# Performance work log

Hardware: AMD Instinct MI355X
Metric: run time of the kernel (lower is better)

## Reference

```python
import jax, jax.numpy as jnp
import numpy as np

TOKENS, D_IN, D_OUT, RANK = 16384, 4096, 4096, 512

def setup_inputs() -> dict:
    key = jax.random.key(0)
    k1, k2, k3, k4 = jax.random.split(key, 4)
    x = jax.random.normal(k1, (TOKENS, D_IN), dtype=jnp.float32)
    U = jax.random.normal(k2, (D_OUT, RANK), dtype=jnp.float32) * 0.02
    sigma = jax.random.uniform(k3, (RANK,), dtype=jnp.float32)
    V = jax.random.normal(k4, (D_IN, RANK), dtype=jnp.float32) * 0.02
    return {"x": x, "U": U, "sigma": sigma, "V": V}

def reference(x, U, sigma, V):
    # W = U @ diag(sigma) @ V.T  (shape [out, in]); out = x @ W.T
    # diag(sigma) contraction expressed as a column scale of U (same math).
    W = (U * sigma[None, :]) @ V.T          # [out, in]
    return x @ W.T                          # [tokens, out]
```

## Files before the change

### kernel.cpp

```cpp
#include <hip/hip_runtime.h>

typedef __bf16 bf16;
typedef __bf16 bf16x4 __attribute__((ext_vector_type(4)));
typedef __bf16 bf16x8 __attribute__((ext_vector_type(8)));
typedef float  f32x4  __attribute__((ext_vector_type(4)));

#define TOKENS 16384
#define D_IN   4096
#define D_OUT  4096
#define RANK   512

__device__ inline void gload_lds16(const void* g, void* l) {
    __builtin_amdgcn_global_load_lds((const __attribute__((address_space(1))) void*)g,
                                     (__attribute__((address_space(3))) void*)l,
                                     16, 0, 0);
}

__global__ __launch_bounds__(256) void vt_scale(const float* __restrict__ V,
                                                const float* __restrict__ sg,
                                                bf16* __restrict__ Vst) {
    __shared__ float tile[64][65];
    const int tx = threadIdx.x & 63;
    const int ty = threadIdx.x >> 6;
    const int kb = blockIdx.x * 64;
    const int rb = blockIdx.y * 64;
    const float s = sg[rb + tx];
#pragma unroll
    for (int i = ty; i < 64; i += 4)
        tile[i][tx] = V[(size_t)(kb + i) * RANK + rb + tx] * s;
    __syncthreads();
#pragma unroll
    for (int i = ty; i < 64; i += 4) {
        int r = rb + i;
        int kp = kb + (tx ^ ((r & 7) << 3));
        Vst[(size_t)r * D_IN + kp] = (bf16)tile[tx][i];
    }
}

__global__ __launch_bounds__(256) void cvt_u_swz(const float* __restrict__ U,
                                                 bf16* __restrict__ Ub) {
    int g = blockIdx.x * 256 + threadIdx.x;
    int n = g >> 6;
    int c = g & 63;
    int blk = c >> 3, q = c & 7;
    const float* src = U + (size_t)n * RANK + c * 8;
    f32x4 v0 = *(const f32x4*)src;
    f32x4 v1 = *(const f32x4*)(src + 4);
    bf16x8 b;
    b[0] = (bf16)v0[0]; b[1] = (bf16)v0[1]; b[2] = (bf16)v0[2]; b[3] = (bf16)v0[3];
    b[4] = (bf16)v1[0]; b[5] = (bf16)v1[1]; b[6] = (bf16)v1[2]; b[7] = (bf16)v1[3];
    *(bf16x8*)(Ub + (size_t)n * RANK + blk * 64 + ((q ^ (n & 7)) * 8)) = b;
}

__device__ inline bf16x8 cvt8(f32x4 a, f32x4 b) {
    bf16x8 r;
    r[0] = (bf16)a[0]; r[1] = (bf16)a[1]; r[2] = (bf16)a[2]; r[3] = (bf16)a[3];
    r[4] = (bf16)b[0]; r[5] = (bf16)b[1]; r[6] = (bf16)b[2]; r[7] = (bf16)b[3];
    return r;
}

__global__ __launch_bounds__(256) void gemm1_alds(const float* __restrict__ A,
                                                  const bf16* __restrict__ B,
                                                  bf16* __restrict__ T,
                                                  int M, int N, int K) {
    __shared__ float Afl[128 * 64];
    __shared__ bf16  Bl[128 * 64];

    const int t  = threadIdx.x;
    const int l  = t & 63;
    const int w  = t >> 6;
    const int wr = w >> 1, wc = w & 1;
    const int lr = l & 15;
    const int kg = l >> 4;
    const int sxorB = (lr & 7) << 3;

    const int nwg = gridDim.x;
    const int bid = blockIdx.x;
    const int cpx = nwg >> 3;
    const int swz = (bid & 7) * cpx + (bid >> 3);
    const int ntn = N >> 7;
    const int tm  = (swz / ntn) << 7;
    const int tn  = (swz % ntn) << 7;

    const int arow = t >> 4;
    const int acr  = t & 15;
    const float* Asrc = A + (size_t)(tm + arow) * K + ((acr ^ arow) << 2);
    const bf16* Bp = B + (size_t)(tn + (t >> 3)) * K + (t & 7) * 8;

    f32x4 acc[4][4] = {};

    for (int kt = 0; kt < K; kt += 64) {
#pragma unroll
        for (int c = 0; c < 8; ++c)
            gload_lds16(Asrc + kt + (size_t)(c * 16) * K, &Afl[(c * 256 + t) * 4]);
#pragma unroll
        for (int c = 0; c < 4; ++c)
            gload_lds16(Bp + kt + (size_t)(c * 32) * K, &Bl[(c * 256 + t) * 8]);
        __syncthreads();

#pragma unroll
        for (int ks = 0; ks < 2; ++ks) {
            bf16x8 af[4], bfr[4];
            const int q0 = ks * 8 + kg * 2;
#pragma unroll
            for (int f = 0; f < 4; ++f) {
                const float* Arow = &Afl[(wr * 64 + f * 16 + lr) * 64];
                f32x4 h0 = *(const f32x4*)&Arow[(q0 ^ lr) << 2];
                f32x4 h1 = *(const f32x4*)&Arow[((q0 + 1) ^ lr) << 2];
                af[f] = cvt8(h0, h1);
                bfr[f] = *(const bf16x8*)&Bl[(wc * 64 + f * 16 + lr) * 64 +
                                             ((ks * 32 + kg * 8) ^ sxorB)];
            }
#pragma unroll
            for (int fm = 0; fm < 4; ++fm)
#pragma unroll
                for (int fn = 0; fn < 4; ++fn)
                    acc[fm][fn] = __builtin_amdgcn_mfma_f32_16x16x32_bf16(
                        af[fm], bfr[fn], acc[fm][fn], 0, 0, 0);
        }
        __syncthreads();
    }

    const int r0 = tm + wr * 64 + kg * 4;
    const int c0 = tn + wc * 64 + lr;
#pragma unroll
    for (int fm = 0; fm < 4; ++fm)
#pragma unroll
        for (int fn = 0; fn < 4; ++fn)
#pragma unroll
            for (int r = 0; r < 4; ++r) {
                int row = r0 + fm * 16 + r;
                int col = (c0 + fn * 16) ^ ((row & 7) << 3);
                T[(size_t)row * N + col] = (bf16)acc[fm][fn][r];
            }
}

__global__ __launch_bounds__(512, 2) void gemm2_8p(const bf16* __restrict__ A,
                                                   const bf16* __restrict__ B,
                                                   float* __restrict__ out,
                                                   int M, int N, int K) {
    __shared__ bf16 Al[2][256 * 64];
    __shared__ bf16 Bl[2][256 * 64];

    const int t   = threadIdx.x;
    const int l   = t & 63;
    const int wid = t >> 6;
    const int wm  = wid >> 2;
    const int wn  = wid & 3;
    const int lr  = l & 15;
    const int kg  = l >> 4;
    const int sxor = (lr & 7) << 3;

    const int nwg = gridDim.x;
    const int bid = blockIdx.x;
    const int cpx = nwg >> 3;
    const int swz = (bid & 7) * cpx + (bid >> 3);
    const int ntn = N >> 8;
    const int tm  = (swz / ntn) << 8;
    const int tn  = (swz % ntn) << 8;

    const bf16* Apt = A + (size_t)(tm + (t >> 3)) * K + (t & 7) * 8;
    const bf16* Bpt = B + (size_t)(tn + (t >> 3)) * K + (t & 7) * 8;
    const int ldst = t * 8;

    const int NT = K >> 6;

    f32x4 acc[8][4] = {};
    bf16x8 aq[4][2], bq[2][2];

#define STAGE(BUF, KT)                                                         \
    _Pragma("unroll") for (int c = 0; c < 4; ++c) {                            \
        gload_lds16(Apt + (KT) + (size_t)(c * 64) * K, &Al[BUF][c * 4096 + ldst]); \
        gload_lds16(Bpt + (KT) + (size_t)(c * 64) * K, &Bl[BUF][c * 4096 + ldst]); \
    }

#define RD_A(BUF, QM)                                                          \
    _Pragma("unroll") for (int f = 0; f < 4; ++f)                              \
    _Pragma("unroll") for (int ks = 0; ks < 2; ++ks)                           \
        aq[f][ks] = *(const bf16x8*)&Al[BUF][(wm * 128 + (QM) * 64 + f * 16 + lr) * 64 + \
                                            ((ks * 32 + kg * 8) ^ sxor)];

#define RD_B(BUF, QN)                                                          \
    _Pragma("unroll") for (int f = 0; f < 2; ++f)                              \
    _Pragma("unroll") for (int ks = 0; ks < 2; ++ks)                           \
        bq[f][ks] = *(const bf16x8*)&Bl[BUF][(wn * 64 + (QN) * 32 + f * 16 + lr) * 64 + \
                                            ((ks * 32 + kg * 8) ^ sxor)];

#define MM(QM, QN)                                                             \
    __builtin_amdgcn_s_setprio(1);                                             \
    _Pragma("unroll") for (int ks = 0; ks < 2; ++ks)                           \
    _Pragma("unroll") for (int fm = 0; fm < 4; ++fm)                           \
    _Pragma("unroll") for (int fn = 0; fn < 2; ++fn)                           \
        acc[(QM) * 4 + fm][(QN) * 2 + fn] = __builtin_amdgcn_mfma_f32_16x16x32_bf16( \
            aq[fm][ks], bq[fn][ks], acc[(QM) * 4 + fm][(QN) * 2 + fn], 0, 0, 0); \
    __builtin_amdgcn_s_setprio(0);

    STAGE(0, 0);
    STAGE(1, 64);
    asm volatile("s_waitcnt vmcnt(8)" ::: "memory");
    __builtin_amdgcn_sched_barrier(0);
    __builtin_amdgcn_s_barrier();
    __builtin_amdgcn_sched_barrier(0);

    for (int i = 0; i < NT; ++i) {
        const int p = i & 1;
        RD_A(p, 0); RD_B(p, 0); MM(0, 0);
        RD_B(p, 1);             MM(0, 1);
        RD_A(p, 1); RD_B(p, 0); MM(1, 0);
        RD_B(p, 1);             MM(1, 1);

        if (i + 1 < NT) {
            __builtin_amdgcn_sched_barrier(0);
            __builtin_amdgcn_s_barrier();
            __builtin_amdgcn_sched_barrier(0);
            if (i + 2 < NT) {
                STAGE(p, (i + 2) * 64);
                asm volatile("s_waitcnt vmcnt(8)" ::: "memory");
            } else {
                asm volatile("s_waitcnt vmcnt(0)" ::: "memory");
            }
            __builtin_amdgcn_sched_barrier(0);
            __builtin_amdgcn_s_barrier();
            __builtin_amdgcn_sched_barrier(0);
        }
    }

    const int r0 = tm + wm * 128 + kg * 4;
    const int c0 = tn + wn * 64 + lr;
#pragma unroll
    for (int fm = 0; fm < 8; ++fm)
#pragma unroll
        for (int fn = 0; fn < 4; ++fn)
#pragma unroll
            for (int r = 0; r < 4; ++r)
                out[(size_t)(r0 + fm * 16 + r) * N + (c0 + fn * 16)] = acc[fm][fn][r];

#undef STAGE
#undef RD_A
#undef RD_B
#undef MM
}

extern "C" void kernel_launch(void* const* d_in, const int* in_sizes, int n_in,
                              void* d_out, int out_size, void* d_ws, size_t ws_size,
                              hipStream_t stream) {
    const float* x  = (const float*)d_in[0];
    const float* U  = (const float*)d_in[1];
    const float* sg = (const float*)d_in[2];
    const float* V  = (const float*)d_in[3];
    float* out = (float*)d_out;

    char* ws = (char*)d_ws;
    bf16* Vst = (bf16*)ws;
    bf16* Ub  = (bf16*)(ws + (4u << 20));
    bf16* T   = (bf16*)(ws + (8u << 20));

    vt_scale<<<dim3(D_IN / 64, RANK / 64), 256, 0, stream>>>(V, sg, Vst);
    cvt_u_swz<<<(D_OUT * RANK / 8) / 256, 256, 0, stream>>>(U, Ub);

    gemm1_alds<<<(TOKENS / 128) * (RANK / 128), 256, 0, stream>>>(
        x, Vst, T, TOKENS, RANK, D_IN);

    gemm2_8p<<<(TOKENS / 256) * (D_OUT / 256), 512, 0, stream>>>(
        T, Ub, out, TOKENS, D_OUT, RANK);
}
```

Before: 250.8 us.

## Rewrite first GEMM as double-buffered 8-wave kernel with 128x256 tiles

Replaces the 4-wave, single-buffered 128x128 first GEMM (x·V·sigma) with an 8-wave kernel that uses a 128x256 tile and double-buffered LDS. Loads for tile i+2 are issued while tile i is computed, with explicit vmcnt waits and barriers, and MFMA blocks run at raised wave priority. The goal is to hide global-load latency and halve the number of times the fp32 x tile is re-read across N. In exchange, LDS use grows to about 96KB, which limits residency to one block per CU, and the grid shrinks to 256 blocks.

```diff
diff --git a/kernel.cpp b/kernel.cpp
--- a/kernel.cpp
+++ b/kernel.cpp
@@ -14,6 +14,13 @@
     __builtin_amdgcn_global_load_lds((const __attribute__((address_space(1))) void*)g,
                                      (__attribute__((address_space(3))) void*)l,
                                      16, 0, 0);
+}
+
+__device__ inline bf16x8 cvt8(f32x4 a, f32x4 b) {
+    bf16x8 r;
+    r[0] = (bf16)a[0]; r[1] = (bf16)a[1]; r[2] = (bf16)a[2]; r[3] = (bf16)a[3];
+    r[4] = (bf16)b[0]; r[5] = (bf16)b[1]; r[6] = (bf16)b[2]; r[7] = (bf16)b[3];
+    return r;
 }
 
 __global__ __launch_bounds__(256) void vt_scale(const float* __restrict__ V,
@@ -52,77 +59,103 @@
     *(bf16x8*)(Ub + (size_t)n * RANK + blk * 64 + ((q ^ (n & 7)) * 8)) = b;
 }
 
-__device__ inline bf16x8 cvt8(f32x4 a, f32x4 b) {
-    bf16x8 r;
-    r[0] = (bf16)a[0]; r[1] = (bf16)a[1]; r[2] = (bf16)a[2]; r[3] = (bf16)a[3];
-    r[4] = (bf16)b[0]; r[5] = (bf16)b[1]; r[6] = (bf16)b[2]; r[7] = (bf16)b[3];
-    return r;
-}
-
-__global__ __launch_bounds__(256) void gemm1_alds(const float* __restrict__ A,
-                                                  const bf16* __restrict__ B,
-                                                  bf16* __restrict__ T,
-                                                  int M, int N, int K) {
-    __shared__ float Afl[128 * 64];
-    __shared__ bf16  Bl[128 * 64];
-
-    const int t  = threadIdx.x;
-    const int l  = t & 63;
-    const int w  = t >> 6;
-    const int wr = w >> 1, wc = w & 1;
-    const int lr = l & 15;
-    const int kg = l >> 4;
+__global__ __launch_bounds__(512, 1) void gemm1_8p(const float* __restrict__ A,
+                                                   const bf16* __restrict__ B,
+                                                   bf16* __restrict__ T,
+                                                   int M, int N, int K) {
+    __shared__ float Afl[2][128 * 64];
+    __shared__ bf16  Bl[2][256 * 64];
+
+    const int t   = threadIdx.x;
+    const int l   = t & 63;
+    const int wid = t >> 6;
+    const int wm  = wid >> 2;
+    const int wn  = wid & 3;
+    const int lr  = l & 15;
+    const int kg  = l >> 4;
     const int sxorB = (lr & 7) << 3;
 
     const int nwg = gridDim.x;
     const int bid = blockIdx.x;
     const int cpx = nwg >> 3;
     const int swz = (bid & 7) * cpx + (bid >> 3);
-    const int ntn = N >> 7;
+    const int ntn = N >> 8;
     const int tm  = (swz / ntn) << 7;
-    const int tn  = (swz % ntn) << 7;
+    const int tn  = (swz % ntn) << 8;
 
     const int arow = t >> 4;
     const int acr  = t & 15;
-    const float* Asrc = A + (size_t)(tm + arow) * K + ((acr ^ arow) << 2);
+    const float* Asrc = A + (size_t)(tm + arow) * K + ((acr ^ (arow & 15)) << 2);
     const bf16* Bp = B + (size_t)(tn + (t >> 3)) * K + (t & 7) * 8;
 
+    const int NT = K >> 6;
+
     f32x4 acc[4][4] = {};
-
-    for (int kt = 0; kt < K; kt += 64) {
-#pragma unroll
-        for (int c = 0; c < 8; ++c)
-            gload_lds16(Asrc + kt + (size_t)(c * 16) * K, &Afl[(c * 256 + t) * 4]);
-#pragma unroll
-        for (int c = 0; c < 4; ++c)
-            gload_lds16(Bp + kt + (size_t)(c * 32) * K, &Bl[(c * 256 + t) * 8]);
-        __syncthreads();
-
-#pragma unroll
-        for (int ks = 0; ks < 2; ++ks) {
-            bf16x8 af[4], bfr[4];
-            const int q0 = ks * 8 + kg * 2;
-#pragma unroll
-            for (int f = 0; f < 4; ++f) {
-                const float* Arow = &Afl[(wr * 64 + f * 16 + lr) * 64];
-                f32x4 h0 = *(const f32x4*)&Arow[(q0 ^ lr) << 2];
-                f32x4 h1 = *(const f32x4*)&Arow[((q0 + 1) ^ lr) << 2];
-                af[f] = cvt8(h0, h1);
-                bfr[f] = *(const bf16x8*)&Bl[(wc * 64 + f * 16 + lr) * 64 +
-                                             ((ks * 32 + kg * 8) ^ sxorB)];
+    bf16x8 aq[2][2], bq[2][2];
+
+#define STAGE1(BUF, KT)                                                        \
+    _Pragma("unroll") for (int c = 0; c < 4; ++c) {                            \
+        gload_lds16(Asrc + (KT) + (size_t)(c * 32) * K, &Afl[BUF][(c * 512 + t) * 4]); \
+        gload_lds16(Bp   + (KT) + (size_t)(c * 64) * K, &Bl[BUF][(c * 512 + t) * 8]);  \
+    }
+
+#define RD_A1(BUF, QM)                                                         \
+    _Pragma("unroll") for (int f = 0; f < 2; ++f)                              \
+    _Pragma("unroll") for (int ks = 0; ks < 2; ++ks) {                         \
+        const float* Arow = &Afl[BUF][(wm * 64 + ((QM) * 2 + f) * 16 + lr) * 64]; \
+        const int q0 = ks * 8 + kg * 2;                                        \
+        f32x4 h0 = *(const f32x4*)&Arow[(q0 ^ lr) << 2];                       \
+        f32x4 h1 = *(const f32x4*)&Arow[((q0 + 1) ^ lr) << 2];                 \
+        aq[f][ks] = cvt8(h0, h1);                                              \
+    }
+
+#define RD_B1(BUF, QN)                                                         \
+    _Pragma("unroll") for (int f = 0; f < 2; ++f)                              \
+    _Pragma("unroll") for (int ks = 0; ks < 2; ++ks)                           \
+        bq[f][ks] = *(const bf16x8*)&Bl[BUF][(wn * 64 + ((QN) * 2 + f) * 16 + lr) * 64 + \
+                                            ((ks * 32 + kg * 8) ^ sxorB)];
+
+#define MM1(QM, QN)                                                            \
+    __builtin_amdgcn_s_setprio(1);                                             \
+    _Pragma("unroll") for (int ks = 0; ks < 2; ++ks)                           \
+    _Pragma("unroll") for (int f = 0; f < 2; ++f)                              \
+    _Pragma("unroll") for (int g = 0; g < 2; ++g)                              \
+        acc[(QM) * 2 + f][(QN) * 2 + g] = __builtin_amdgcn_mfma_f32_16x16x32_bf16( \
+            aq[f][ks], bq[g][ks], acc[(QM) * 2 + f][(QN) * 2 + g], 0, 0, 0);   \
+    __builtin_amdgcn_s_setprio(0);
+
+    STAGE1(0, 0);
+    STAGE1(1, 64);
+    asm volatile("s_waitcnt vmcnt(8)" ::: "memory");
+    __builtin_amdgcn_sched_barrier(0);
+    __builtin_amdgcn_s_barrier();
+    __builtin_amdgcn_sched_barrier(0);
+
+    for (int i = 0; i < NT; ++i) {
+        const int p = i & 1;
+        RD_A1(p, 0); RD_B1(p, 0); MM1(0, 0);
+        RD_B1(p, 1);              MM1(0, 1);
+        RD_A1(p, 1); RD_B1(p, 0); MM1(1, 0);
+        RD_B1(p, 1);              MM1(1, 1);
+
+        if (i + 1 < NT) {
+            __builtin_amdgcn_sched_barrier(0);
+            __builtin_amdgcn_s_barrier();
+            __builtin_amdgcn_sched_barrier(0);
+            if (i + 2 < NT) {
+                STAGE1(p, (i + 2) * 64);
+                asm volatile("s_waitcnt vmcnt(8)" ::: "memory");
+            } else {
+                asm volatile("s_waitcnt vmcnt(0)" ::: "memory");
             }
-#pragma unroll
-            for (int fm = 0; fm < 4; ++fm)
-#pragma unroll
-                for (int fn = 0; fn < 4; ++fn)
-                    acc[fm][fn] = __builtin_amdgcn_mfma_f32_16x16x32_bf16(
-                        af[fm], bfr[fn], acc[fm][fn], 0, 0, 0);
+            __builtin_amdgcn_sched_barrier(0);
+            __builtin_amdgcn_s_barrier();
+            __builtin_amdgcn_sched_barrier(0);
         }
-        __syncthreads();
-    }
-
-    const int r0 = tm + wr * 64 + kg * 4;
-    const int c0 = tn + wc * 64 + lr;
+    }
+
+    const int r0 = tm + wm * 64 + kg * 4;
+    const int c0 = tn + wn * 64 + lr;
 #pragma unroll
     for (int fm = 0; fm < 4; ++fm)
 #pragma unroll
@@ -133,6 +166,10 @@
                 int col = (c0 + fn * 16) ^ ((row & 7) << 3);
                 T[(size_t)row * N + col] = (bf16)acc[fm][fn][r];
             }
+#undef STAGE1
+#undef RD_A1
+#undef RD_B1
+#undef MM1
 }
 
 __global__ __launch_bounds__(512, 2) void gemm2_8p(const bf16* __restrict__ A,
@@ -258,7 +295,7 @@
     vt_scale<<<dim3(D_IN / 64, RANK / 64), 256, 0, stream>>>(V, sg, Vst);
     cvt_u_swz<<<(D_OUT * RANK / 8) / 256, 256, 0, stream>>>(U, Ub);
 
-    gemm1_alds<<<(TOKENS / 128) * (RANK / 128), 256, 0, stream>>>(
+    gemm1_8p<<<(TOKENS / 128) * (RANK / 256), 512, 0, stream>>>(
         x, Vst, T, TOKENS, RANK, D_IN);
 
     gemm2_8p<<<(TOKENS / 256) * (D_OUT / 256), 512, 0, stream>>>(
```

After: 269.8 us. 7.6% more time.

## Split-K gemm1 with 256x256 tiles, bf16 LDS staging and separate reduction

Applied to the files above, without the earlier changes.

Replaces the 128x128 first GEMM with a 256x256-tile, 512-thread kernel that splits K=4096 into four 1024-wide slices. Each slice writes a bf16 partial product, and a new reduce kernel sums the partials and writes the swizzled T layout. The x tile is now loaded through registers and converted to bf16 once before the LDS store, instead of being staged as fp32 and converted on every fragment read. This raises per-tile data reuse and keeps the grid large, at the cost of extra partial-buffer traffic, an additional launch, and summing bf16-rounded partials.

```diff
diff --git a/kernel.cpp b/kernel.cpp
--- a/kernel.cpp
+++ b/kernel.cpp
@@ -52,87 +52,107 @@
     *(bf16x8*)(Ub + (size_t)n * RANK + blk * 64 + ((q ^ (n & 7)) * 8)) = b;
 }
 
-__device__ inline bf16x8 cvt8(f32x4 a, f32x4 b) {
-    bf16x8 r;
-    r[0] = (bf16)a[0]; r[1] = (bf16)a[1]; r[2] = (bf16)a[2]; r[3] = (bf16)a[3];
-    r[4] = (bf16)b[0]; r[5] = (bf16)b[1]; r[6] = (bf16)b[2]; r[7] = (bf16)b[3];
-    return r;
-}
-
-__global__ __launch_bounds__(256) void gemm1_alds(const float* __restrict__ A,
-                                                  const bf16* __restrict__ B,
-                                                  bf16* __restrict__ T,
-                                                  int M, int N, int K) {
-    __shared__ float Afl[128 * 64];
-    __shared__ bf16  Bl[128 * 64];
-
-    const int t  = threadIdx.x;
-    const int l  = t & 63;
-    const int w  = t >> 6;
-    const int wr = w >> 1, wc = w & 1;
-    const int lr = l & 15;
-    const int kg = l >> 4;
-    const int sxorB = (lr & 7) << 3;
+__global__ __launch_bounds__(512) void gemm1_v2(const float* __restrict__ A,
+                                                const bf16* __restrict__ B,
+                                                bf16* __restrict__ P,
+                                                int M, int N, int Kfull) {
+    __shared__ bf16 Al[256 * 64];
+    __shared__ bf16 Bl[256 * 64];
+
+    const int t   = threadIdx.x;
+    const int l   = t & 63;
+    const int wid = t >> 6;
+    const int wm  = wid >> 2;
+    const int wn  = wid & 3;
+    const int lr  = l & 15;
+    const int kg  = l >> 4;
 
     const int nwg = gridDim.x;
     const int bid = blockIdx.x;
     const int cpx = nwg >> 3;
     const int swz = (bid & 7) * cpx + (bid >> 3);
-    const int ntn = N >> 7;
-    const int tm  = (swz / ntn) << 7;
-    const int tn  = (swz % ntn) << 7;
+    const int split = swz >> 7;
+    const int tile  = swz & 127;
+    const int tm    = (tile >> 1) << 8;
+    const int tn    = (tile & 1) << 8;
+    const int kbase = split << 10;
+    const int Ks    = 1024;
 
     const int arow = t >> 4;
-    const int acr  = t & 15;
-    const float* Asrc = A + (size_t)(tm + arow) * K + ((acr ^ arow) << 2);
-    const bf16* Bp = B + (size_t)(tn + (t >> 3)) * K + (t & 7) * 8;
-
-    f32x4 acc[4][4] = {};
-
-    for (int kt = 0; kt < K; kt += 64) {
+    const int acg  = t & 15;
+    const float* Ap = A + (size_t)(tm + arow) * Kfull + kbase + acg * 4;
+    const int awo = (((acg >> 1) ^ (arow & 7)) << 3) + ((acg & 1) << 2);
+    const bf16* Bp = B + (size_t)(tn + (t >> 3)) * Kfull + kbase + (t & 7) * 8;
+
+    f32x4 acc[8][4] = {};
+
+    for (int kt = 0; kt < Ks; kt += 64) {
+#pragma unroll
+        for (int c = 0; c < 4; ++c)
+            gload_lds16(Bp + kt + (size_t)(c * 64) * Kfull, &Bl[(c * 512 + t) * 8]);
+        f32x4 ra[8];
 #pragma unroll
         for (int c = 0; c < 8; ++c)
-            gload_lds16(Asrc + kt + (size_t)(c * 16) * K, &Afl[(c * 256 + t) * 4]);
-#pragma unroll
-        for (int c = 0; c < 4; ++c)
-            gload_lds16(Bp + kt + (size_t)(c * 32) * K, &Bl[(c * 256 + t) * 8]);
+            ra[c] = *(const f32x4*)(Ap + kt + (size_t)(c * 32) * Kfull);
+#pragma unroll
+        for (int c = 0; c < 8; ++c) {
+            bf16x4 b = { (bf16)ra[c][0], (bf16)ra[c][1], (bf16)ra[c][2], (bf16)ra[c][3] };
+            *(bf16x4*)&Al[(c * 32 + arow) * 64 + awo] = b;
+        }
         __syncthreads();
 
 #pragma unroll
         for (int ks = 0; ks < 2; ++ks) {
-            bf16x8 af[4], bfr[4];
-            const int q0 = ks * 8 + kg * 2;
-#pragma unroll
-            for (int f = 0; f < 4; ++f) {
-                const float* Arow = &Afl[(wr * 64 + f * 16 + lr) * 64];
-                f32x4 h0 = *(const f32x4*)&Arow[(q0 ^ lr) << 2];
-                f32x4 h1 = *(const f32x4*)&Arow[((q0 + 1) ^ lr) << 2];
-                af[f] = cvt8(h0, h1);
-                bfr[f] = *(const bf16x8*)&Bl[(wc * 64 + f * 16 + lr) * 64 +
-                                             ((ks * 32 + kg * 8) ^ sxorB)];
-            }
-#pragma unroll
-            for (int fm = 0; fm < 4; ++fm)
+            const int gx = ((ks * 4 + kg) ^ (lr & 7)) << 3;
+            bf16x8 bq[4];
+#pragma unroll
+            for (int fn = 0; fn < 4; ++fn)
+                bq[fn] = *(const bf16x8*)&Bl[(wn * 64 + fn * 16 + lr) * 64 + gx];
+#pragma unroll
+            for (int fm = 0; fm < 8; ++fm) {
+                bf16x8 aq = *(const bf16x8*)&Al[(wm * 128 + fm * 16 + lr) * 64 + gx];
 #pragma unroll
                 for (int fn = 0; fn < 4; ++fn)
                     acc[fm][fn] = __builtin_amdgcn_mfma_f32_16x16x32_bf16(
-                        af[fm], bfr[fn], acc[fm][fn], 0, 0, 0);
+                        aq, bq[fn], acc[fm][fn], 0, 0, 0);
+            }
         }
         __syncthreads();
     }
 
-    const int r0 = tm + wr * 64 + kg * 4;
-    const int c0 = tn + wc * 64 + lr;
-#pragma unroll
-    for (int fm = 0; fm < 4; ++fm)
+    bf16* Po = P + (size_t)split * M * N;
+    const int r0 = tm + wm * 128 + kg * 4;
+    const int c0 = tn + wn * 64 + lr;
+#pragma unroll
+    for (int fm = 0; fm < 8; ++fm)
 #pragma unroll
         for (int fn = 0; fn < 4; ++fn)
 #pragma unroll
-            for (int r = 0; r < 4; ++r) {
-                int row = r0 + fm * 16 + r;
-                int col = (c0 + fn * 16) ^ ((row & 7) << 3);
-                T[(size_t)row * N + col] = (bf16)acc[fm][fn][r];
-            }
+            for (int r = 0; r < 4; ++r)
+                Po[(size_t)(r0 + fm * 16 + r) * N + (c0 + fn * 16)] = (bf16)acc[fm][fn][r];
+}
+
+__global__ __launch_bounds__(256) void reduce_T(const bf16* __restrict__ P,
+                                                bf16* __restrict__ T) {
+    const size_t slab = (size_t)TOKENS * RANK;
+    const int ng = TOKENS * (RANK / 8);
+    const int stride = gridDim.x * 256;
+    for (int i = blockIdx.x * 256 + threadIdx.x; i < ng; i += stride) {
+        int row = i >> 6;
+        int g   = i & 63;
+        float s[8] = {0, 0, 0, 0, 0, 0, 0, 0};
+#pragma unroll
+        for (int sp = 0; sp < 4; ++sp) {
+            bf16x8 v = *(const bf16x8*)&P[sp * slab + (size_t)i * 8];
+#pragma unroll
+            for (int j = 0; j < 8; ++j) s[j] += (float)v[j];
+        }
+        bf16x8 o;
+#pragma unroll
+        for (int j = 0; j < 8; ++j) o[j] = (bf16)s[j];
+        int blk = g >> 3, q = g & 7;
+        *(bf16x8*)&T[(size_t)row * RANK + blk * 64 + ((q ^ (row & 7)) * 8)] = o;
+    }
 }
 
 __global__ __launch_bounds__(512, 2) void gemm2_8p(const bf16* __restrict__ A,
@@ -254,12 +274,14 @@
     bf16* Vst = (bf16*)ws;
     bf16* Ub  = (bf16*)(ws + (4u << 20));
     bf16* T   = (bf16*)(ws + (8u << 20));
+    bf16* P   = (bf16*)(ws + (32u << 20));
 
     vt_scale<<<dim3(D_IN / 64, RANK / 64), 256, 0, stream>>>(V, sg, Vst);
     cvt_u_swz<<<(D_OUT * RANK / 8) / 256, 256, 0, stream>>>(U, Ub);
 
-    gemm1_alds<<<(TOKENS / 128) * (RANK / 128), 256, 0, stream>>>(
-        x, Vst, T, TOKENS, RANK, D_IN);
+    gemm1_v2<<<512, 512, 0, stream>>>(x, Vst, P, TOKENS, RANK, D_IN);
+
+    reduce_T<<<2048, 256, 0, stream>>>(P, T);
 
     gemm2_8p<<<(TOKENS / 256) * (D_OUT / 256), 512, 0, stream>>>(
         T, Ub, out, TOKENS, D_OUT, RANK);
```

After: 278.8 us. 11.1% more time.
